# Performance work log

Hardware: AMD Instinct MI355X
Metric: run time of the kernel (lower is better)

Reference implementation:

```python
import jax, jax.numpy as jnp
import numpy as np

N_HEADS = 8
TANH_CLIP = 10.0
NEG_INF = -1e9


def setup_inputs() -> dict:
    key = jax.random.key(0)
    ks = jax.random.split(key, 5)
    B, G, D = 64, 640, 256
    scale = 1.0 / np.sqrt(D)
    return {
        "embeddings": jax.random.normal(ks[0], (B, G, D), dtype=jnp.float32),
        "W_node": jax.random.normal(ks[1], (D, 3 * D), dtype=jnp.float32) * scale,
        "W_fixed": jax.random.normal(ks[2], (D, D), dtype=jnp.float32) * scale,
        "W_step": jax.random.normal(ks[3], (D, D), dtype=jnp.float32) * scale,
        "W_out": jax.random.normal(ks[4], (D, D), dtype=jnp.float32) * scale,
        "n_steps": 512,
    }


def reference(embeddings, W_node, W_fixed, W_step, W_out, n_steps):
    B, G, D = embeddings.shape
    H = N_HEADS
    dh = D // H

    # _precompute: fixed context + glimpse K/V and logit K
    graph_embed = embeddings.mean(axis=1)                      # [B, D]
    fixed_ctx = graph_embed @ W_fixed                          # [B, D]
    kvl = embeddings @ W_node                                  # [B, G, 3D]
    g_key, g_val, logit_key = jnp.split(kvl, 3, axis=-1)
    g_key = g_key.reshape(B, G, H, dh).transpose(0, 2, 1, 3)   # [B, H, G, dh]
    g_val = g_val.reshape(B, G, H, dh).transpose(0, 2, 1, 3)   # [B, H, G, dh]

    inv_sqrt_dh = 1.0 / np.sqrt(dh)
    inv_sqrt_D = 1.0 / np.sqrt(D)

    def step(carry, _):
        visited, prev_embed = carry                            # [B, G] bool, [B, D]
        # step context query (first step uses graph embedding)
        q = fixed_ctx + prev_embed @ W_step                    # [B, D]
        q_h = q.reshape(B, H, dh)                              # [B, H, dh]
        # masked glimpse attention
        compat = jnp.einsum('bhd,bhgd->bhg', q_h, g_key) * inv_sqrt_dh
        compat = jnp.where(visited[:, None, :], NEG_INF, compat)
        attn = jax.nn.softmax(compat, axis=-1)                 # [B, H, G]
        heads = jnp.einsum('bhg,bhgd->bhd', attn, g_val)       # [B, H, dh]
        glimpse = heads.reshape(B, D) @ W_out                  # [B, D]
        # single-head logits with tanh clipping
        logits = jnp.einsum('bd,bgd->bg', glimpse, logit_key) * inv_sqrt_D
        logits = TANH_CLIP * jnp.tanh(logits)
        logits = jnp.where(visited, NEG_INF, logits)
        log_p = jax.nn.log_softmax(logits, axis=-1)            # [B, G]
        # greedy selection, update state
        selected = jnp.argmax(log_p, axis=-1)                  # [B]
        visited = visited | jax.nn.one_hot(selected, G, dtype=jnp.bool_)
        prev_embed = jnp.take_along_axis(
            embeddings, selected[:, None, None], axis=1)[:, 0, :]
        return (visited, prev_embed), (log_p, selected)

    init = (jnp.zeros((B, G), dtype=jnp.bool_), graph_embed)
    _, (log_ps, sels) = jax.lax.scan(step, init, None, length=n_steps)
    log_p_all = log_ps.transpose(1, 0, 2)                      # [B, T, G]
    pi = sels.transpose(1, 0)                                  # [B, T]
    return log_p_all, pi
```

## Files before the change

kernel.cpp:

```cpp
#include <hip/hip_runtime.h>
#include <math.h>

#define B_ 64
#define G_ 640
#define D_ 256
#define H_ 8
#define DH_ 32
#define NBLK 4
#define TPB 512
#define GVL 512
#define GVSTR 516
#define NEG_INF_F (-1e9f)

__device__ __constant__ float INV_SQRT_DH = 0.17677669529663687f;
__device__ __constant__ float INV_SQRT_D  = 0.0625f;

__global__ __launch_bounds__(256) void precompute_ctx(
    const float* __restrict__ emb, const float* __restrict__ W_fixed,
    const float* __restrict__ W_step, float* __restrict__ fixed_ctx,
    float* __restrict__ q0)
{
  const int b = blockIdx.x, d = threadIdx.x;
  __shared__ float ge[D_];
  const float* eb = emb + (size_t)b * G_ * D_;
  float s = 0.f;
  for (int g = 0; g < G_; ++g) s += eb[(size_t)g * D_ + d];
  ge[d] = s * (1.0f / (float)G_);
  __syncthreads();
  float fc = 0.f, qq = 0.f;
  for (int k = 0; k < D_; ++k) {
    const float gk = ge[k];
    fc = fmaf(gk, W_fixed[k * D_ + d], fc);
    qq = fmaf(gk, W_step[k * D_ + d], qq);
  }
  fixed_ctx[b * D_ + d] = fc;
  q0[b * D_ + d] = fc + qq;
}

__global__ __launch_bounds__(256) void build_bmat(
    const float* __restrict__ W_node, const float* __restrict__ W_step,
    const float* __restrict__ W_out, float* __restrict__ Bmat)
{
  const int k = blockIdx.x, t = threadIdx.x;
  __shared__ float wn3[D_];
  wn3[t] = W_node[k * 768 + 512 + t];
  __syncthreads();
  Bmat[k * 1024 + t]       = W_node[k * 768 + t];
  Bmat[k * 1024 + 256 + t] = W_node[k * 768 + 256 + t];
  float acc = 0.f;
  for (int j = 0; j < D_; ++j) acc = fmaf(wn3[j], W_out[t * D_ + j], acc);
  Bmat[k * 1024 + 512 + t] = acc;
  Bmat[k * 1024 + 768 + t] = W_step[k * D_ + t];
}

__global__ __launch_bounds__(256) void gemm_scatter(
    const float* __restrict__ A, const float* __restrict__ Bm,
    const float* __restrict__ fixed_ctx,
    float* __restrict__ gkT, float* __restrict__ gv,
    float* __restrict__ lk2T, float* __restrict__ q_all)
{
  __shared__ float As[16][132];
  __shared__ float Bs[16][132];
  const int tid = threadIdx.x;
  const int bm = blockIdx.x;
  const int bn = blockIdx.y;
  const int tr = tid / 16, tc = tid % 16;
  const int row0 = bm * 128, col0 = bn * 128;
  float acc[8][8];
#pragma unroll
  for (int i = 0; i < 8; ++i)
#pragma unroll
    for (int j = 0; j < 8; ++j) acc[i][j] = 0.f;

  for (int k0 = 0; k0 < D_; k0 += 16) {
#pragma unroll
    for (int s = tid; s < 512; s += 256) {
      const int r = s >> 2, c4 = (s & 3) * 4;
      const float4 v = *(const float4*)&A[(size_t)(row0 + r) * D_ + k0 + c4];
      As[c4 + 0][r] = v.x; As[c4 + 1][r] = v.y;
      As[c4 + 2][r] = v.z; As[c4 + 3][r] = v.w;
    }
#pragma unroll
    for (int s = tid; s < 512; s += 256) {
      const int r = s >> 5, c4 = (s & 31) * 4;
      *(float4*)&Bs[r][c4] = *(const float4*)&Bm[(size_t)(k0 + r) * 1024 + col0 + c4];
    }
    __syncthreads();
#pragma unroll
    for (int kk = 0; kk < 16; ++kk) {
      float a[8], bfr[8];
#pragma unroll
      for (int i = 0; i < 8; ++i) a[i] = As[kk][tr * 8 + i];
#pragma unroll
      for (int j = 0; j < 8; ++j) bfr[j] = Bs[kk][tc * 8 + j];
#pragma unroll
      for (int i = 0; i < 8; ++i)
#pragma unroll
        for (int j = 0; j < 8; ++j) acc[i][j] = fmaf(a[i], bfr[j], acc[i][j]);
    }
    __syncthreads();
  }

#pragma unroll
  for (int i = 0; i < 8; ++i) {
    const int row = row0 + tr * 8 + i;
    const int bb = row / G_;
    const int g = row - bb * G_;
#pragma unroll
    for (int j = 0; j < 8; ++j) {
      const int n = col0 + tc * 8 + j;
      const float v = acc[i][j];
      if (n < 256) {
        const int h = n >> 5, d = n & 31;
        gkT[(((size_t)bb * H_ + h) * DH_ + d) * G_ + g] = v;
      } else if (n < 512) {
        const int m2 = n - 256, h = m2 >> 5, d = m2 & 31;
        gv[(((size_t)bb * H_ + h) * G_ + g) * DH_ + d] = v;
      } else if (n < 768) {
        const int d = n - 512;
        lk2T[((size_t)bb * D_ + d) * G_ + g] = v;
      } else {
        const int d = n - 768;
        q_all[((size_t)(bb * G_ + g)) * D_ + d] = v + fixed_ctx[bb * D_ + d];
      }
    }
  }
}

__global__ __launch_bounds__(TPB, 2) void step_headsplit(
    const float* __restrict__ gkT, const float* __restrict__ gv,
    const float* __restrict__ lk2T, const float* __restrict__ q_all,
    const float* __restrict__ q0, const int* __restrict__ n_steps_p,
    float* __restrict__ comm1, unsigned int* __restrict__ bar,
    float* __restrict__ out)
{
  const int x = blockIdx.x;
  const int b   = ((x >> 5) << 3) | (x & 7);
  const int blk = (x >> 3) & 3;
  const int t = threadIdx.x;
  const int T = *n_steps_p;
  const int h0 = blk * 2;
  const int d0 = blk * 64;
  float* out_logp = out;
  float* out_pi   = out + (size_t)B_ * T * G_;

  __shared__ __align__(16) float gv_lds[2 * DH_ * GVSTR];
  __shared__ __align__(16) float attn_s[2 * G_];
  __shared__ __align__(16) float plog_l[G_];
  __shared__ float logits_s[G_];
  __shared__ int   vis[G_];
  __shared__ float hpart[8][64];
  __shared__ float esum_p[8][2];
  __shared__ float heads_s[64];
  __shared__ float q_s[64];
  __shared__ float redv[8]; __shared__ int redi[8]; __shared__ float reds[8];
  __shared__ int   sel_s;
  __shared__ float lse_s;

  const int lane = t & 63, wave = t >> 6;
  const int qt  = t & 3;
  const int oct = t & 7;
  const int part3 = t >> 6;
  const int hd3 = t & 63;
  const int hh3 = hd3 >> 5, dd3 = hd3 & 31;

  float gk_r[10][8];
#pragma unroll
  for (int k = 0; k < 10; ++k) {
    const int p = k * 128 + (t >> 2);
    const int hh = (p >= G_) ? 1 : 0;
    const int g = p - hh * G_;
    const float* src = gkT + (((size_t)b * H_ + h0 + hh) * DH_ + qt * 8) * G_ + g;
#pragma unroll
    for (int j = 0; j < 8; ++j) gk_r[k][j] = src[(size_t)j * G_];
  }
  float lk_r[10][8];
#pragma unroll
  for (int k = 0; k < 10; ++k) {
    const int g = k * 64 + (t >> 3);
    const float* src = lk2T + ((size_t)b * D_ + d0 + oct * 8) * G_ + g;
#pragma unroll
    for (int j = 0; j < 8; ++j) lk_r[k][j] = src[(size_t)j * G_];
  }
  for (int idx = t; idx < 2 * GVL * DH_; idx += TPB) {
    const int d = idx & 31, g = (idx >> 5) & (GVL - 1), hh = idx >> 14;
    gv_lds[(hh * DH_ + d) * GVSTR + g] =
        gv[(((size_t)b * H_ + h0 + hh) * G_ + g) * DH_ + d];
  }
  float gv_r[16];
  {
    const float* src = gv + (((size_t)b * H_ + h0 + hh3) * G_ + GVL + part3 * 16) * DH_ + dd3;
#pragma unroll
    for (int i = 0; i < 16; ++i) gv_r[i] = src[(size_t)i * DH_];
  }

  for (int idx = t; idx < G_; idx += TPB) vis[idx] = 0;
  if (t == 0) sel_s = 0;
  __syncthreads();

  unsigned int* mybar = bar + b * 32;

  for (int step = 0; step < T; ++step) {
    const float* qsrc = (step == 0) ? (q0 + (size_t)b * D_)
                                    : (q_all + ((size_t)b * G_ + sel_s) * D_);
    if (t < 64) q_s[t] = qsrc[d0 + t];
    __syncthreads();

    float qreg[2][8];
#pragma unroll
    for (int hh = 0; hh < 2; ++hh)
#pragma unroll
      for (int j = 0; j < 8; ++j) qreg[hh][j] = q_s[hh * 32 + qt * 8 + j];
#pragma unroll
    for (int k = 0; k < 10; ++k) {
      const int p = k * 128 + (t >> 2);
      const int hh = (p >= G_) ? 1 : 0;
      const int g = p - hh * G_;
      float a = 0.f;
#pragma unroll
      for (int j = 0; j < 8; ++j) a = fmaf(qreg[hh][j], gk_r[k][j], a);
      a += __shfl_xor(a, 1);
      a += __shfl_xor(a, 2);
      if (qt == 0) attn_s[hh * G_ + g] = vis[g] ? 0.f : expf(a * INV_SQRT_DH);
    }
    __syncthreads();

    {
      const float* gvrow = &gv_lds[(hh3 * DH_ + dd3) * GVSTR];
      const float* arow = &attn_s[hh3 * G_];
      float acc = 0.f, es = 0.f;
      const int gA = part3 * 64;
#pragma unroll
      for (int i = 0; i < 16; ++i) {
        const float4 ev = *(const float4*)&arow[gA + i * 4];
        const float4 gvv = *(const float4*)&gvrow[gA + i * 4];
        acc = fmaf(ev.x, gvv.x, acc); acc = fmaf(ev.y, gvv.y, acc);
        acc = fmaf(ev.z, gvv.z, acc); acc = fmaf(ev.w, gvv.w, acc);
        if (dd3 == 0) es += ev.x + ev.y + ev.z + ev.w;
      }
      const int gB = GVL + part3 * 16;
#pragma unroll
      for (int i = 0; i < 16; ++i) {
        const float e = arow[gB + i];
        acc = fmaf(e, gv_r[i], acc);
        if (dd3 == 0) es += e;
      }
      hpart[part3][hd3] = acc;
      if (dd3 == 0) esum_p[part3][hh3] = es;
    }
    __syncthreads();
    if (t < 64) {
      float num = 0.f, den = 0.f;
#pragma unroll
      for (int p = 0; p < 8; ++p) num += hpart[p][t];
#pragma unroll
      for (int p = 0; p < 8; ++p) den += esum_p[p][t >> 5];
      heads_s[t] = num / den;
    }
    __syncthreads();

    float hreg[8];
#pragma unroll
    for (int j = 0; j < 8; ++j) hreg[j] = heads_s[oct * 8 + j];
#pragma unroll
    for (int k = 0; k < 10; ++k) {
      float a = 0.f;
#pragma unroll
      for (int j = 0; j < 8; ++j) a = fmaf(hreg[j], lk_r[k][j], a);
      a += __shfl_xor(a, 1);
      a += __shfl_xor(a, 2);
      a += __shfl_xor(a, 4);
      if (oct == 0) plog_l[k * 64 + (t >> 3)] = a;
    }
    __syncthreads();

    float* myslot = comm1 + (((size_t)b * 2 + (step & 1)) * NBLK + blk) * G_;
    for (int idx = t; idx < G_; idx += TPB)
      __hip_atomic_store(&myslot[idx], plog_l[idx], __ATOMIC_RELAXED, __HIP_MEMORY_SCOPE_AGENT);
    __syncthreads();
    if (t == 0) {
      __hip_atomic_fetch_add(mybar, 1u, __ATOMIC_RELEASE, __HIP_MEMORY_SCOPE_AGENT);
      const unsigned tgt = (unsigned)(step + 1) * NBLK;
      while (__hip_atomic_load(mybar, __ATOMIC_ACQUIRE, __HIP_MEMORY_SCOPE_AGENT) < tgt)
        __builtin_amdgcn_s_sleep(2);
    }
    __syncthreads();

    const float* cbase = comm1 + ((size_t)b * 2 + (step & 1)) * NBLK * G_;
    for (int idx = t; idx < G_; idx += TPB) {
      float s = 0.f;
#pragma unroll
      for (int kk = 0; kk < NBLK; ++kk)
        s += __hip_atomic_load(&cbase[kk * G_ + idx], __ATOMIC_RELAXED, __HIP_MEMORY_SCOPE_AGENT);
      float lg = 10.0f * tanhf(s * INV_SQRT_D);
      if (vis[idx]) lg = NEG_INF_F;
      logits_s[idx] = lg;
    }
    __syncthreads();

    {
      float v = logits_s[t]; int vi = t;
      float es = expf(v - 10.0f);
      if (t < G_ - TPB) {
        const float v2 = logits_s[TPB + t];
        es += expf(v2 - 10.0f);
        if (v2 > v) { v = v2; vi = TPB + t; }
      }
#pragma unroll
      for (int off = 32; off; off >>= 1) {
        const float ov = __shfl_down(v, off);
        const int oi = __shfl_down(vi, off);
        const float oe = __shfl_down(es, off);
        es += oe;
        if (ov > v || (ov == v && oi < vi)) { v = ov; vi = oi; }
      }
      if (lane == 0) { redv[wave] = v; redi[wave] = vi; reds[wave] = es; }
    }
    __syncthreads();
    if (t == 0) {
      float mv = redv[0]; int mi = redi[0]; float ss = reds[0];
      for (int w = 1; w < 8; ++w) {
        ss += reds[w];
        if (redv[w] > mv || (redv[w] == mv && redi[w] < mi)) { mv = redv[w]; mi = redi[w]; }
      }
      sel_s = mi;
      lse_s = 10.0f + logf(ss);
      vis[mi] = 1;
      if (blk == 0) out_pi[(size_t)b * T + step] = (float)mi;
    }
    __syncthreads();

    if (t < 160)
      out_logp[((size_t)b * T + step) * G_ + blk * 160 + t] =
          logits_s[blk * 160 + t] - lse_s;
  }
}

extern "C" void kernel_launch(void* const* d_in, const int* in_sizes, int n_in,
                              void* d_out, int out_size, void* d_ws, size_t ws_size,
                              hipStream_t stream)
{
  const float* emb     = (const float*)d_in[0];
  const float* W_node  = (const float*)d_in[1];
  const float* W_fixed = (const float*)d_in[2];
  const float* W_step  = (const float*)d_in[3];
  const float* W_out   = (const float*)d_in[4];
  const int*   n_steps = (const int*)d_in[5];

  float* ws = (float*)d_ws;
  float* fixed_ctx = ws;
  float* q0        = fixed_ctx + B_ * D_;
  float* Bmat      = q0 + B_ * D_;
  float* gkT       = Bmat + D_ * 1024;
  float* gv        = gkT + (size_t)B_ * D_ * G_;
  float* lk2T      = gv + (size_t)B_ * D_ * G_;
  float* q_all     = lk2T + (size_t)B_ * D_ * G_;
  float* comm1     = q_all + (size_t)B_ * G_ * D_;
  unsigned int* bar = (unsigned int*)(comm1 + (size_t)B_ * 2 * NBLK * G_);

  hipMemsetAsync(bar, 0, B_ * 32 * sizeof(unsigned int), stream);
  precompute_ctx<<<B_, 256, 0, stream>>>(emb, W_fixed, W_step, fixed_ctx, q0);
  build_bmat<<<D_, 256, 0, stream>>>(W_node, W_step, W_out, Bmat);
  gemm_scatter<<<dim3(320, 8), 256, 0, stream>>>(emb, Bmat, fixed_ctx,
                                                 gkT, gv, lk2T, q_all);
  step_headsplit<<<B_ * NBLK, TPB, 0, stream>>>(gkT, gv, lk2T, q_all, q0, n_steps,
                                                comm1, bar, (float*)d_out);
}
```

Baseline: 7.271 ms.

## Replace all-to-all step barrier with master-worker mailbox for logits reduction

Drops the per-step atomic counter barrier, where all four blocks per batch row summed every partial and ran softmax/argmax redundantly. Now blocks 1-3 publish their partial logits plus a step flag, and block 0 alone reduces, selects, and writes all outputs. Block 0 then posts a packed step/selection word that the workers spin on. This is meant to shorten the synchronisation handshake, but it serialises output writes and the reduction onto one block and relies on relaxed system-scope atomics with no explicit release/acquire ordering.

```diff
diff --git a/kernel.cpp b/kernel.cpp
--- a/kernel.cpp
+++ b/kernel.cpp
@@ -127,11 +127,13 @@
   }
 }
 
-__global__ __launch_bounds__(TPB, 2) void step_headsplit(
+__global__ __launch_bounds__(TPB, 2) void step_mailbox(
     const float* __restrict__ gkT, const float* __restrict__ gv,
     const float* __restrict__ lk2T, const float* __restrict__ q_all,
     const float* __restrict__ q0, const int* __restrict__ n_steps_p,
-    float* __restrict__ comm1, unsigned int* __restrict__ bar,
+    float* __restrict__ partials,
+    unsigned int* __restrict__ flags,
+    unsigned int* __restrict__ selw,
     float* __restrict__ out)
 {
   const int x = blockIdx.x;
@@ -198,7 +200,9 @@
   if (t == 0) sel_s = 0;
   __syncthreads();
 
-  unsigned int* mybar = bar + b * 32;
+  unsigned int* myflags = flags + b * 8;
+  unsigned int* myselw  = selw + b * 32;
+  float* pb = partials + (size_t)b * 3 * G_;
 
   for (int step = 0; step < T; ++step) {
     const float* qsrc = (step == 0) ? (q0 + (size_t)b * D_)
@@ -274,65 +278,93 @@
     }
     __syncthreads();
 
-    float* myslot = comm1 + (((size_t)b * 2 + (step & 1)) * NBLK + blk) * G_;
-    for (int idx = t; idx < G_; idx += TPB)
-      __hip_atomic_store(&myslot[idx], plog_l[idx], __ATOMIC_RELAXED, __HIP_MEMORY_SCOPE_AGENT);
-    __syncthreads();
-    if (t == 0) {
-      __hip_atomic_fetch_add(mybar, 1u, __ATOMIC_RELEASE, __HIP_MEMORY_SCOPE_AGENT);
-      const unsigned tgt = (unsigned)(step + 1) * NBLK;
-      while (__hip_atomic_load(mybar, __ATOMIC_ACQUIRE, __HIP_MEMORY_SCOPE_AGENT) < tgt)
-        __builtin_amdgcn_s_sleep(2);
-    }
-    __syncthreads();
-
-    const float* cbase = comm1 + ((size_t)b * 2 + (step & 1)) * NBLK * G_;
-    for (int idx = t; idx < G_; idx += TPB) {
-      float s = 0.f;
-#pragma unroll
-      for (int kk = 0; kk < NBLK; ++kk)
-        s += __hip_atomic_load(&cbase[kk * G_ + idx], __ATOMIC_RELAXED, __HIP_MEMORY_SCOPE_AGENT);
-      float lg = 10.0f * tanhf(s * INV_SQRT_D);
-      if (vis[idx]) lg = NEG_INF_F;
-      logits_s[idx] = lg;
-    }
-    __syncthreads();
-
-    {
-      float v = logits_s[t]; int vi = t;
-      float es = expf(v - 10.0f);
-      if (t < G_ - TPB) {
-        const float v2 = logits_s[TPB + t];
-        es += expf(v2 - 10.0f);
-        if (v2 > v) { v = v2; vi = TPB + t; }
-      }
-#pragma unroll
-      for (int off = 32; off; off >>= 1) {
-        const float ov = __shfl_down(v, off);
-        const int oi = __shfl_down(vi, off);
-        const float oe = __shfl_down(es, off);
-        es += oe;
-        if (ov > v || (ov == v && oi < vi)) { v = ov; vi = oi; }
-      }
-      if (lane == 0) { redv[wave] = v; redi[wave] = vi; reds[wave] = es; }
-    }
-    __syncthreads();
-    if (t == 0) {
-      float mv = redv[0]; int mi = redi[0]; float ss = reds[0];
-      for (int w = 1; w < 8; ++w) {
-        ss += reds[w];
-        if (redv[w] > mv || (redv[w] == mv && redi[w] < mi)) { mv = redv[w]; mi = redi[w]; }
-      }
-      sel_s = mi;
-      lse_s = 10.0f + logf(ss);
-      vis[mi] = 1;
-      if (blk == 0) out_pi[(size_t)b * T + step] = (float)mi;
-    }
-    __syncthreads();
-
-    if (t < 160)
-      out_logp[((size_t)b * T + step) * G_ + blk * 160 + t] =
-          logits_s[blk * 160 + t] - lse_s;
+    if (blk != 0) {
+      float* myp = pb + (size_t)(blk - 1) * G_;
+      for (int idx = t; idx < G_; idx += TPB)
+        __hip_atomic_store(&myp[idx], plog_l[idx], __ATOMIC_RELAXED,
+                           __HIP_MEMORY_SCOPE_SYSTEM);
+      __syncthreads();
+      if (t == 0) {
+        __hip_atomic_store(&myflags[blk], (unsigned)(step + 1), __ATOMIC_RELAXED,
+                           __HIP_MEMORY_SCOPE_SYSTEM);
+        const unsigned tgt = (unsigned)(step + 1) << 10;
+        unsigned w;
+        while ((w = __hip_atomic_load(&myselw[0], __ATOMIC_RELAXED,
+                                      __HIP_MEMORY_SCOPE_SYSTEM)) < tgt)
+          __builtin_amdgcn_s_sleep(1);
+        const int mi = (int)(w & 1023u);
+        sel_s = mi;
+        vis[mi] = 1;
+      }
+      __syncthreads();
+    } else {
+      if (t == 0) {
+        const unsigned tg = (unsigned)(step + 1);
+        for (;;) {
+          const unsigned f1 = __hip_atomic_load(&myflags[1], __ATOMIC_RELAXED,
+                                                __HIP_MEMORY_SCOPE_SYSTEM);
+          const unsigned f2 = __hip_atomic_load(&myflags[2], __ATOMIC_RELAXED,
+                                                __HIP_MEMORY_SCOPE_SYSTEM);
+          const unsigned f3 = __hip_atomic_load(&myflags[3], __ATOMIC_RELAXED,
+                                                __HIP_MEMORY_SCOPE_SYSTEM);
+          if (f1 >= tg && f2 >= tg && f3 >= tg) break;
+          __builtin_amdgcn_s_sleep(1);
+        }
+      }
+      __syncthreads();
+
+      for (int idx = t; idx < G_; idx += TPB) {
+        float s = plog_l[idx];
+        s += __hip_atomic_load(&pb[idx], __ATOMIC_RELAXED, __HIP_MEMORY_SCOPE_SYSTEM);
+        s += __hip_atomic_load(&pb[G_ + idx], __ATOMIC_RELAXED, __HIP_MEMORY_SCOPE_SYSTEM);
+        s += __hip_atomic_load(&pb[2 * G_ + idx], __ATOMIC_RELAXED, __HIP_MEMORY_SCOPE_SYSTEM);
+        float lg = 10.0f * tanhf(s * INV_SQRT_D);
+        if (vis[idx]) lg = NEG_INF_F;
+        logits_s[idx] = lg;
+      }
+      __syncthreads();
+
+      {
+        float v = logits_s[t]; int vi = t;
+        float es = expf(v - 10.0f);
+        if (t < G_ - TPB) {
+          const float v2 = logits_s[TPB + t];
+          es += expf(v2 - 10.0f);
+          if (v2 > v) { v = v2; vi = TPB + t; }
+        }
+#pragma unroll
+        for (int off = 32; off; off >>= 1) {
+          const float ov = __shfl_down(v, off);
+          const int oi = __shfl_down(vi, off);
+          const float oe = __shfl_down(es, off);
+          es += oe;
+          if (ov > v || (ov == v && oi < vi)) { v = ov; vi = oi; }
+        }
+        if (lane == 0) { redv[wave] = v; redi[wave] = vi; reds[wave] = es; }
+      }
+      __syncthreads();
+      if (t == 0) {
+        float mv = redv[0]; int mi = redi[0]; float ss = reds[0];
+        for (int w = 1; w < 8; ++w) {
+          ss += reds[w];
+          if (redv[w] > mv || (redv[w] == mv && redi[w] < mi)) { mv = redv[w]; mi = redi[w]; }
+        }
+        sel_s = mi;
+        __hip_atomic_store(&myselw[0], ((unsigned)(step + 1) << 10) | (unsigned)mi,
+                           __ATOMIC_RELAXED, __HIP_MEMORY_SCOPE_SYSTEM);
+        lse_s = 10.0f + logf(ss);
+        vis[mi] = 1;
+        __builtin_nontemporal_store((float)mi, &out_pi[(size_t)b * T + step]);
+      }
+      __syncthreads();
+
+      {
+        const float ls = lse_s;
+        float* orow = out_logp + ((size_t)b * T + step) * G_;
+        for (int idx = t; idx < G_; idx += TPB)
+          __builtin_nontemporal_store(logits_s[idx] - ls, &orow[idx]);
+      }
+    }
   }
 }
 
@@ -355,14 +387,15 @@
   float* gv        = gkT + (size_t)B_ * D_ * G_;
   float* lk2T      = gv + (size_t)B_ * D_ * G_;
   float* q_all     = lk2T + (size_t)B_ * D_ * G_;
-  float* comm1     = q_all + (size_t)B_ * G_ * D_;
-  unsigned int* bar = (unsigned int*)(comm1 + (size_t)B_ * 2 * NBLK * G_);
-
-  hipMemsetAsync(bar, 0, B_ * 32 * sizeof(unsigned int), stream);
+  float* partials  = q_all + (size_t)B_ * G_ * D_;
+  unsigned int* flags = (unsigned int*)(partials + (size_t)B_ * 3 * G_);
+  unsigned int* selw  = flags + B_ * 8;
+
+  hipMemsetAsync(flags, 0, (B_ * 8 + B_ * 32) * sizeof(unsigned int), stream);
   precompute_ctx<<<B_, 256, 0, stream>>>(emb, W_fixed, W_step, fixed_ctx, q0);
   build_bmat<<<D_, 256, 0, stream>>>(W_node, W_step, W_out, Bmat);
   gemm_scatter<<<dim3(320, 8), 256, 0, stream>>>(emb, Bmat, fixed_ctx,
                                                  gkT, gv, lk2T, q_all);
-  step_headsplit<<<B_ * NBLK, TPB, 0, stream>>>(gkT, gv, lk2T, q_all, q0, n_steps,
-                                                comm1, bar, (float*)d_out);
+  step_mailbox<<<B_ * NBLK, TPB, 0, stream>>>(gkT, gv, lk2T, q_all, q0, n_steps,
+                                              partials, flags, selw, (float*)d_out);
 }
```

Result: faster. 6.013 ms (-17.3%).

## Replace partial-logit reduction barrier with tagged all-to-all head and argmax exchange

Applied to the files above, without the earlier changes.

Each of the four blocks per batch row now publishes its 64 head values as tagged 64-bit words and polls the other blocks' values. It then computes full-dimension logits for only its own 160 nodes, where before it wrote partial logits over all 640 nodes to a global scratch and waited on an atomic counter barrier. The cross-block argmax and softmax-sum are exchanged the same way, through small tagged max/index/sum records. This replaces a counter barrier plus 640x4 float global traffic per step with two small flag-in-data exchanges, and splits the tanh/softmax work across blocks. In exchange it adds a second spin wait per step and uses system-scope atomics.

```diff
diff --git a/kernel.cpp b/kernel.cpp
--- a/kernel.cpp
+++ b/kernel.cpp
@@ -127,11 +127,12 @@
   }
 }
 
-__global__ __launch_bounds__(TPB, 2) void step_headsplit(
+__global__ __launch_bounds__(TPB, 2) void step_a2a(
     const float* __restrict__ gkT, const float* __restrict__ gv,
     const float* __restrict__ lk2T, const float* __restrict__ q_all,
     const float* __restrict__ q0, const int* __restrict__ n_steps_p,
-    float* __restrict__ comm1, unsigned int* __restrict__ bar,
+    unsigned long long* __restrict__ hm,
+    unsigned long long* __restrict__ sm,
     float* __restrict__ out)
 {
   const int x = blockIdx.x;
@@ -141,28 +142,31 @@
   const int T = *n_steps_p;
   const int h0 = blk * 2;
   const int d0 = blk * 64;
+  const int gq0 = blk * 160;
   float* out_logp = out;
   float* out_pi   = out + (size_t)B_ * T * G_;
 
   __shared__ __align__(16) float gv_lds[2 * DH_ * GVSTR];
   __shared__ __align__(16) float attn_s[2 * G_];
-  __shared__ __align__(16) float plog_l[G_];
-  __shared__ float logits_s[G_];
+  __shared__ float heads_s[D_];
+  __shared__ float lraw_s[160];
+  __shared__ float logits_s[160];
   __shared__ int   vis[G_];
   __shared__ float hpart[8][64];
   __shared__ float esum_p[8][2];
-  __shared__ float heads_s[64];
   __shared__ float q_s[64];
-  __shared__ float redv[8]; __shared__ int redi[8]; __shared__ float reds[8];
+  __shared__ float redv[3]; __shared__ int redi[3]; __shared__ float reds[3];
+  __shared__ unsigned long long stage[8];
   __shared__ int   sel_s;
   __shared__ float lse_s;
 
   const int lane = t & 63, wave = t >> 6;
   const int qt  = t & 3;
-  const int oct = t & 7;
   const int part3 = t >> 6;
   const int hd3 = t & 63;
   const int hh3 = hd3 >> 5, dd3 = hd3 & 31;
+  const int col = t & 31;
+  const int row = t >> 5;
 
   float gk_r[10][8];
 #pragma unroll
@@ -177,8 +181,8 @@
   float lk_r[10][8];
 #pragma unroll
   for (int k = 0; k < 10; ++k) {
-    const int g = k * 64 + (t >> 3);
-    const float* src = lk2T + ((size_t)b * D_ + d0 + oct * 8) * G_ + g;
+    const int g = gq0 + k * 16 + row;
+    const float* src = lk2T + ((size_t)b * D_ + col * 8) * G_ + g;
 #pragma unroll
     for (int j = 0; j < 8; ++j) lk_r[k][j] = src[(size_t)j * G_];
   }
@@ -198,9 +202,12 @@
   if (t == 0) sel_s = 0;
   __syncthreads();
 
-  unsigned int* mybar = bar + b * 32;
+  unsigned long long* myhm = hm + (size_t)b * NBLK * 64;
+  unsigned long long* mysm = sm + (size_t)b * NBLK * 2;
 
   for (int step = 0; step < T; ++step) {
+    const unsigned tag = (unsigned)(step + 1);
+
     const float* qsrc = (step == 0) ? (q0 + (size_t)b * D_)
                                     : (q_all + ((size_t)b * G_ + sel_s) * D_);
     if (t < 64) q_s[t] = qsrc[d0 + t];
@@ -255,13 +262,30 @@
       for (int p = 0; p < 8; ++p) num += hpart[p][t];
 #pragma unroll
       for (int p = 0; p < 8; ++p) den += esum_p[p][t >> 5];
-      heads_s[t] = num / den;
+      heads_s[d0 + t] = num / den;
+    }
+    __syncthreads();
+
+    if (t < 64) {
+      const unsigned long long w =
+          ((unsigned long long)tag << 32) |
+          (unsigned long long)__float_as_uint(heads_s[d0 + t]);
+      __hip_atomic_store(&myhm[blk * 64 + t], w, __ATOMIC_RELAXED,
+                         __HIP_MEMORY_SCOPE_SYSTEM);
+    } else if (t < 256) {
+      const int rb = (blk + (t >> 6)) & 3;
+      const int i = t & 63;
+      unsigned long long w;
+      while ((unsigned)((w = __hip_atomic_load(&myhm[rb * 64 + i], __ATOMIC_RELAXED,
+                                               __HIP_MEMORY_SCOPE_SYSTEM)) >> 32) < tag)
+        __builtin_amdgcn_s_sleep(1);
+      heads_s[rb * 64 + i] = __uint_as_float((unsigned)w);
     }
     __syncthreads();
 
     float hreg[8];
 #pragma unroll
-    for (int j = 0; j < 8; ++j) hreg[j] = heads_s[oct * 8 + j];
+    for (int j = 0; j < 8; ++j) hreg[j] = heads_s[col * 8 + j];
 #pragma unroll
     for (int k = 0; k < 10; ++k) {
       float a = 0.f;
@@ -270,69 +294,80 @@
       a += __shfl_xor(a, 1);
       a += __shfl_xor(a, 2);
       a += __shfl_xor(a, 4);
-      if (oct == 0) plog_l[k * 64 + (t >> 3)] = a;
-    }
-    __syncthreads();
-
-    float* myslot = comm1 + (((size_t)b * 2 + (step & 1)) * NBLK + blk) * G_;
-    for (int idx = t; idx < G_; idx += TPB)
-      __hip_atomic_store(&myslot[idx], plog_l[idx], __ATOMIC_RELAXED, __HIP_MEMORY_SCOPE_AGENT);
-    __syncthreads();
-    if (t == 0) {
-      __hip_atomic_fetch_add(mybar, 1u, __ATOMIC_RELEASE, __HIP_MEMORY_SCOPE_AGENT);
-      const unsigned tgt = (unsigned)(step + 1) * NBLK;
-      while (__hip_atomic_load(mybar, __ATOMIC_ACQUIRE, __HIP_MEMORY_SCOPE_AGENT) < tgt)
-        __builtin_amdgcn_s_sleep(2);
-    }
-    __syncthreads();
-
-    const float* cbase = comm1 + ((size_t)b * 2 + (step & 1)) * NBLK * G_;
-    for (int idx = t; idx < G_; idx += TPB) {
-      float s = 0.f;
-#pragma unroll
-      for (int kk = 0; kk < NBLK; ++kk)
-        s += __hip_atomic_load(&cbase[kk * G_ + idx], __ATOMIC_RELAXED, __HIP_MEMORY_SCOPE_AGENT);
-      float lg = 10.0f * tanhf(s * INV_SQRT_D);
-      if (vis[idx]) lg = NEG_INF_F;
-      logits_s[idx] = lg;
+      a += __shfl_xor(a, 8);
+      a += __shfl_xor(a, 16);
+      if (col == 0) lraw_s[k * 16 + row] = a;
     }
     __syncthreads();
 
     {
-      float v = logits_s[t]; int vi = t;
-      float es = expf(v - 10.0f);
-      if (t < G_ - TPB) {
-        const float v2 = logits_s[TPB + t];
-        es += expf(v2 - 10.0f);
-        if (v2 > v) { v = v2; vi = TPB + t; }
-      }
-#pragma unroll
-      for (int off = 32; off; off >>= 1) {
-        const float ov = __shfl_down(v, off);
-        const int oi = __shfl_down(vi, off);
-        const float oe = __shfl_down(es, off);
-        es += oe;
-        if (ov > v || (ov == v && oi < vi)) { v = ov; vi = oi; }
-      }
-      if (lane == 0) { redv[wave] = v; redi[wave] = vi; reds[wave] = es; }
-    }
-    __syncthreads();
+      float lval = -INFINITY, eval = 0.f;
+      int gidx = 1 << 30;
+      if (t < 160) {
+        float lg = 10.0f * tanhf(lraw_s[t] * INV_SQRT_D);
+        if (vis[gq0 + t]) lg = NEG_INF_F;
+        logits_s[t] = lg;
+        lval = lg; gidx = gq0 + t;
+        eval = expf(lg - 10.0f);
+      }
+      if (t < 192) {
+        float v = lval; int vi = gidx; float es = eval;
+#pragma unroll
+        for (int off = 32; off; off >>= 1) {
+          const float ov = __shfl_down(v, off);
+          const int oi = __shfl_down(vi, off);
+          const float oe = __shfl_down(es, off);
+          es += oe;
+          if (ov > v || (ov == v && oi < vi)) { v = ov; vi = oi; }
+        }
+        if (lane == 0) { redv[wave] = v; redi[wave] = vi; reds[wave] = es; }
+      }
+    }
+    __syncthreads();
+
     if (t == 0) {
       float mv = redv[0]; int mi = redi[0]; float ss = reds[0];
-      for (int w = 1; w < 8; ++w) {
+      for (int w = 1; w < 3; ++w) {
         ss += reds[w];
         if (redv[w] > mv || (redv[w] == mv && redi[w] < mi)) { mv = redv[w]; mi = redi[w]; }
+      }
+      const unsigned long long w0 =
+          ((unsigned long long)((tag << 16) | (unsigned)mi) << 32) |
+          (unsigned long long)__float_as_uint(mv);
+      const unsigned long long w1 =
+          ((unsigned long long)(tag << 16) << 32) |
+          (unsigned long long)__float_as_uint(ss);
+      __hip_atomic_store(&mysm[blk * 2 + 0], w0, __ATOMIC_RELAXED, __HIP_MEMORY_SCOPE_SYSTEM);
+      __hip_atomic_store(&mysm[blk * 2 + 1], w1, __ATOMIC_RELAXED, __HIP_MEMORY_SCOPE_SYSTEM);
+    }
+    if (t < 8) {
+      unsigned long long w;
+      while ((unsigned)((w = __hip_atomic_load(&mysm[t], __ATOMIC_RELAXED,
+                                               __HIP_MEMORY_SCOPE_SYSTEM)) >> 48) < tag)
+        __builtin_amdgcn_s_sleep(1);
+      stage[t] = w;
+    }
+    __syncthreads();
+    if (t == 0) {
+      float mv = -INFINITY; int mi = 1 << 30; float ss = 0.f;
+#pragma unroll
+      for (int k = 0; k < NBLK; ++k) {
+        const unsigned long long w0 = stage[2 * k], w1 = stage[2 * k + 1];
+        const float v = __uint_as_float((unsigned)w0);
+        const int vi = (int)((w0 >> 32) & 0xFFFFu);
+        ss += __uint_as_float((unsigned)w1);
+        if (v > mv || (v == mv && vi < mi)) { mv = v; mi = vi; }
       }
       sel_s = mi;
       lse_s = 10.0f + logf(ss);
       vis[mi] = 1;
-      if (blk == 0) out_pi[(size_t)b * T + step] = (float)mi;
+      if (blk == 0) __builtin_nontemporal_store((float)mi, &out_pi[(size_t)b * T + step]);
     }
     __syncthreads();
 
     if (t < 160)
-      out_logp[((size_t)b * T + step) * G_ + blk * 160 + t] =
-          logits_s[blk * 160 + t] - lse_s;
+      __builtin_nontemporal_store(logits_s[t] - lse_s,
+          &out_logp[((size_t)b * T + step) * G_ + gq0 + t]);
   }
 }
 
@@ -355,14 +390,14 @@
   float* gv        = gkT + (size_t)B_ * D_ * G_;
   float* lk2T      = gv + (size_t)B_ * D_ * G_;
   float* q_all     = lk2T + (size_t)B_ * D_ * G_;
-  float* comm1     = q_all + (size_t)B_ * G_ * D_;
-  unsigned int* bar = (unsigned int*)(comm1 + (size_t)B_ * 2 * NBLK * G_);
-
-  hipMemsetAsync(bar, 0, B_ * 32 * sizeof(unsigned int), stream);
+  unsigned long long* hm = (unsigned long long*)(q_all + (size_t)B_ * G_ * D_);
+  unsigned long long* sm = hm + (size_t)B_ * NBLK * 64;
+
+  hipMemsetAsync(hm, 0, (size_t)(B_ * NBLK * 64 + B_ * NBLK * 2) * sizeof(unsigned long long), stream);
   precompute_ctx<<<B_, 256, 0, stream>>>(emb, W_fixed, W_step, fixed_ctx, q0);
   build_bmat<<<D_, 256, 0, stream>>>(W_node, W_step, W_out, Bmat);
   gemm_scatter<<<dim3(320, 8), 256, 0, stream>>>(emb, Bmat, fixed_ctx,
                                                  gkT, gv, lk2T, q_all);
-  step_headsplit<<<B_ * NBLK, TPB, 0, stream>>>(gkT, gv, lk2T, q_all, q0, n_steps,
-                                                comm1, bar, (float*)d_out);
+  step_a2a<<<B_ * NBLK, TPB, 0, stream>>>(gkT, gv, lk2T, q_all, q0, n_steps,
+                                          hm, sm, (float*)d_out);
 }
```

Measured after the change: 6.192 ms. 14.8% less time.
